# Performance work log

Hardware: AMD Instinct MI355X
Metric: run time of the kernel (lower is better)

## Reference

```python
import jax, jax.numpy as jnp
import numpy as np

B, C, H, W, NMAX = 16, 1, 128, 8192, 64


def setup_inputs() -> dict:
    key = jax.random.key(0)
    x = jax.random.normal(key, (B, C, H, W), dtype=jnp.float32)
    # Build realistic non-overlapping, sorted chirp boundaries with numpy.
    rng = np.random.default_rng(0)
    slot = W // NMAX  # 128 columns per chirp slot
    gaps = rng.integers(0, 40, size=(B, NMAX))
    widths = rng.integers(20, slot - 40, size=(B, NMAX))
    starts = np.arange(NMAX)[None, :] * slot + gaps
    ends = starts + widths
    n = rng.integers(48, NMAX + 1, size=(B,)).astype(np.int32)
    xi = np.stack([starts, ends], axis=-1).astype(np.int32)
    valid = np.arange(NMAX)[None, :] < n[:, None]
    xi = xi * valid[:, :, None]  # zero out invalid rows
    return {
        "x": x,
        "xi": jnp.asarray(xi),
        "N": jnp.asarray(n),
        "sep_param": jnp.zeros((1, 1, 1), dtype=jnp.float32),  # learned sep token scalar
    }


def reference(x, xi, N, sep_param):
    """Vectorized TinyBird.compactify_data: remove silence between chirp
    blocks, packing blocks contiguously with 1-column separators.
    Returns (x_new, xi_new). x_new keeps full width W (original truncates
    to data-dependent w_max; padding beyond w_max is zeros, same values)."""
    Bb, Cc, Hh, Ww = x.shape
    nmax = xi.shape[1]
    idx = jnp.arange(nmax, dtype=jnp.int32)[None, :]            # (1, Nmax)
    Nc = N.reshape(Bb, 1).astype(jnp.int32)                      # (B, 1)
    w = jnp.clip(xi[:, :, 1] - xi[:, :, 0], 0, None).astype(jnp.int32)
    valid = idx < Nc                                             # (B, Nmax)
    wv = jnp.where(valid, w, 0)
    csum = jnp.cumsum(wv, axis=1)
    start_new = csum - wv + idx                                  # compressed starts
    end_new = csum + idx                                         # compressed ends
    xi_new = jnp.where(valid[:, :, None],
                       jnp.stack([start_new, end_new], axis=-1), 0).astype(xi.dtype)

    # For every output column j, find which compressed segment it falls in.
    j = jnp.arange(Ww, dtype=jnp.int32)
    big = jnp.int32(Ww + nmax + 2)
    start_search = jnp.where(valid, start_new, big)              # keep sorted
    seg = jax.vmap(lambda s: jnp.searchsorted(s, j, side='right'))(start_search) - 1
    seg = jnp.clip(seg, 0, nmax - 1)                             # (B, W)
    bidx = jnp.arange(Bb)[:, None]
    s_new = start_new[bidx, seg]
    e_new = end_new[bidx, seg]
    seg_valid = valid[bidx, seg]
    in_seg = seg_valid & (j[None, :] >= s_new) & (j[None, :] < e_new)
    is_sep = seg_valid & (j[None, :] == e_new) & (seg < (Nc - 1))
    src = jnp.clip(xi[bidx, seg, 0].astype(jnp.int32) + (j[None, :] - s_new), 0, Ww - 1)
    src_full = jnp.broadcast_to(src[:, None, None, :], (Bb, Cc, Hh, Ww))
    gathered = jnp.take_along_axis(x, src_full, axis=3)          # ragged gather
    sep_val = sep_param[0, 0, 0]                                 # sep_token column value
    x_new = jnp.where(in_seg[:, None, None, :], gathered,
                      jnp.where(is_sep[:, None, None, :], sep_val, jnp.float32(0)))
    return x_new, xi_new
```

## Files before the change

kernel.cpp:

```cpp
#include <hip/hip_runtime.h>

#define Bn 16
#define Hn 128
#define Wn 8192
#define NMAX 64
#define TILE 1024
#define TPB 256

__global__ void xi_new_kernel(const int* __restrict__ xi,
                              const int* __restrict__ N,
                              float* __restrict__ out_xi) {
    int b = blockIdx.x;
    int i = threadIdx.x;
    int nb = N[b];
    int s0 = xi[(b * NMAX + i) * 2 + 0];
    int s1 = xi[(b * NMAX + i) * 2 + 1];
    int w = s1 - s0; if (w < 0) w = 0;
    bool valid = i < nb;
    int wv = valid ? w : 0;
    int c = wv;
    #pragma unroll
    for (int d = 1; d < 64; d <<= 1) {
        int t = __shfl_up(c, d, 64);
        if (i >= d) c += t;
    }
    int start_new = c - wv + i;
    int end_new = c + i;
    out_xi[(b * NMAX + i) * 2 + 0] = valid ? (float)start_new : 0.0f;
    out_xi[(b * NMAX + i) * 2 + 1] = valid ? (float)end_new : 0.0f;
}

__global__ __launch_bounds__(TPB) void compact_kernel(
    const float* __restrict__ x, const int* __restrict__ xi,
    const int* __restrict__ N, const float* __restrict__ sep_param,
    float* __restrict__ out) {
    __shared__ int s_start[NMAX];
    __shared__ int s_end[NMAX];
    __shared__ int s_src0[NMAX];
    __shared__ int s_n;

    const int blk  = blockIdx.x;
    const int tile = blk & 7;
    const int row  = blk >> 3;
    const int b    = row >> 7;
    const int tid  = threadIdx.x;

    if (tid < NMAX) {
        int nb = N[b];
        int s0 = xi[(b * NMAX + tid) * 2 + 0];
        int s1 = xi[(b * NMAX + tid) * 2 + 1];
        int w = s1 - s0; if (w < 0) w = 0;
        bool valid = tid < nb;
        int wv = valid ? w : 0;
        int c = wv;
        #pragma unroll
        for (int d = 1; d < 64; d <<= 1) {
            int t = __shfl_up(c, d, 64);
            if (tid >= d) c += t;
        }
        int start_new = c - wv + tid;
        int end_new = c + tid;
        s_start[tid] = valid ? start_new : 0x7FFFFFFF;
        s_end[tid]   = valid ? end_new : -1;
        s_src0[tid]  = s0;
        if (tid == 0) s_n = nb;
    }
    __syncthreads();

    const float sep = sep_param[0];
    const int nb = s_n;
    const float* __restrict__ xrow = x + (size_t)row * Wn;
    float* __restrict__ orow = out + (size_t)row * Wn;
    const int j0 = tile * TILE + tid * 4;

    float arr[4];
    #pragma unroll
    for (int k = 0; k < 4; ++k) {
        const int j = j0 + k;
        int seg = 0;
        #pragma unroll
        for (int step = 32; step > 0; step >>= 1) {
            int cand = seg + step;
            if (cand < NMAX && s_start[cand] <= j) seg = cand;
        }
        const int s = s_start[seg];
        const int e = s_end[seg];
        float val = 0.0f;
        if (j < e) {
            int src = s_src0[seg] + (j - s);
            if (src < 0) src = 0;
            if (src > Wn - 1) src = Wn - 1;
            val = xrow[src];
        } else if (j == e && seg < nb - 1) {
            val = sep;
        }
        arr[k] = val;
    }
    *reinterpret_cast<float4*>(orow + j0) = make_float4(arr[0], arr[1], arr[2], arr[3]);
}

extern "C" void kernel_launch(void* const* d_in, const int* in_sizes, int n_in,
                              void* d_out, int out_size, void* d_ws, size_t ws_size,
                              hipStream_t stream) {
    const float* x   = (const float*)d_in[0];
    const int* xi    = (const int*)d_in[1];
    const int* N     = (const int*)d_in[2];
    const float* sep = (const float*)d_in[3];

    float* out_x  = (float*)d_out;
    float* out_xi = (float*)d_out + (size_t)Bn * Hn * Wn;

    xi_new_kernel<<<Bn, NMAX, 0, stream>>>(xi, N, out_xi);

    const int blocks = Bn * Hn * (Wn / TILE);
    compact_kernel<<<blocks, TPB, 0, stream>>>(x, xi, N, sep, out_x);
}
```

Before: 137.3 us.

## Precompute per-batch source index map once, then run a lightweight row gather

A new code_kernel runs the segment scan and binary search once per batch element and per column. It writes an int map to workspace holding the source column, or a marker for separator or zero, and also emits xi_new. A gather_kernel then processes one full row per block, reading that map and gathering from x, so the per-row prefix scan, shared-memory setup, barrier and binary search are no longer repeated for each of the 128 rows. This adds a 512KB workspace round trip and a second launch, and falls back to the old path if the workspace is too small.

```diff
diff --git a/kernel.cpp b/kernel.cpp
--- a/kernel.cpp
+++ b/kernel.cpp
@@ -4,8 +4,170 @@
 #define Hn 128
 #define Wn 8192
 #define NMAX 64
-#define TILE 1024
-#define TPB 256
+
+__global__ __launch_bounds__(256) void code_kernel(
+    const int* __restrict__ xi, const int* __restrict__ N,
+    int* __restrict__ code, float* __restrict__ out_xi) {
+    __shared__ int s_start[NMAX];
+    __shared__ int s_end[NMAX];
+    __shared__ int s_src0[NMAX];
+    __shared__ int s_n;
+
+    const int b    = blockIdx.x >> 3;
+    const int tile = blockIdx.x & 7;
+    const int tid  = threadIdx.x;
+
+    if (tid < NMAX) {
+        int nb = N[b];
+        int s0 = xi[(b * NMAX + tid) * 2 + 0];
+        int s1 = xi[(b * NMAX + tid) * 2 + 1];
+        int w = s1 - s0; if (w < 0) w = 0;
+        bool valid = tid < nb;
+        int wv = valid ? w : 0;
+        int c = wv;
+        #pragma unroll
+        for (int d = 1; d < 64; d <<= 1) {
+            int t = __shfl_up(c, d, 64);
+            if (tid >= d) c += t;
+        }
+        int start_new = c - wv + tid;
+        int end_new = c + tid;
+        s_start[tid] = valid ? start_new : 0x7FFFFFFF;
+        s_end[tid]   = valid ? end_new : -1;
+        s_src0[tid]  = s0;
+        if (tid == 0) s_n = nb;
+        if (tile == 0) {
+            out_xi[(b * NMAX + tid) * 2 + 0] = valid ? (float)start_new : 0.0f;
+            out_xi[(b * NMAX + tid) * 2 + 1] = valid ? (float)end_new : 0.0f;
+        }
+    }
+    __syncthreads();
+
+    const int nb = s_n;
+    const int j0 = tile * 1024 + tid * 4;
+    int out4[4];
+    #pragma unroll
+    for (int k = 0; k < 4; ++k) {
+        const int j = j0 + k;
+        int seg = 0;
+        #pragma unroll
+        for (int step = 32; step > 0; step >>= 1) {
+            int cand = seg + step;
+            if (cand < NMAX && s_start[cand] <= j) seg = cand;
+        }
+        const int s = s_start[seg];
+        const int e = s_end[seg];
+        int c;
+        if (j < e) {
+            int src = s_src0[seg] + (j - s);
+            if (src < 0) src = 0;
+            if (src > Wn - 1) src = Wn - 1;
+            c = src;
+        } else if (j == e && seg < nb - 1) {
+            c = -2;
+        } else {
+            c = -1;
+        }
+        out4[k] = c;
+    }
+    *reinterpret_cast<int4*>(code + b * Wn + j0) =
+        make_int4(out4[0], out4[1], out4[2], out4[3]);
+}
+
+__global__ __launch_bounds__(256) void gather_kernel(
+    const float* __restrict__ x, const int* __restrict__ code,
+    const float* __restrict__ sep_param, float* __restrict__ out) {
+    const int row = blockIdx.x;
+    const int b   = row >> 7;
+    const int tid = threadIdx.x;
+
+    const float sep = sep_param[0];
+    const float* __restrict__ xrow = x + (size_t)row * Wn;
+    float* __restrict__ orow = out + (size_t)row * Wn;
+    const int* __restrict__ crow = code + b * Wn;
+
+    int4 c[8];
+    #pragma unroll
+    for (int g = 0; g < 8; ++g) {
+        c[g] = *reinterpret_cast<const int4*>(crow + g * 1024 + tid * 4);
+    }
+    #pragma unroll
+    for (int g = 0; g < 8; ++g) {
+        float4 v;
+        v.x = (c[g].x >= 0) ? xrow[c[g].x] : ((c[g].x == -2) ? sep : 0.0f);
+        v.y = (c[g].y >= 0) ? xrow[c[g].y] : ((c[g].y == -2) ? sep : 0.0f);
+        v.z = (c[g].z >= 0) ? xrow[c[g].z] : ((c[g].z == -2) ? sep : 0.0f);
+        v.w = (c[g].w >= 0) ? xrow[c[g].w] : ((c[g].w == -2) ? sep : 0.0f);
+        *reinterpret_cast<float4*>(orow + g * 1024 + tid * 4) = v;
+    }
+}
+
+__global__ __launch_bounds__(256) void compact_kernel(
+    const float* __restrict__ x, const int* __restrict__ xi,
+    const int* __restrict__ N, const float* __restrict__ sep_param,
+    float* __restrict__ out) {
+    __shared__ int s_start[NMAX];
+    __shared__ int s_end[NMAX];
+    __shared__ int s_src0[NMAX];
+    __shared__ int s_n;
+
+    const int blk  = blockIdx.x;
+    const int tile = blk & 7;
+    const int row  = blk >> 3;
+    const int b    = row >> 7;
+    const int tid  = threadIdx.x;
+
+    if (tid < NMAX) {
+        int nb = N[b];
+        int s0 = xi[(b * NMAX + tid) * 2 + 0];
+        int s1 = xi[(b * NMAX + tid) * 2 + 1];
+        int w = s1 - s0; if (w < 0) w = 0;
+        bool valid = tid < nb;
+        int wv = valid ? w : 0;
+        int c = wv;
+        #pragma unroll
+        for (int d = 1; d < 64; d <<= 1) {
+            int t = __shfl_up(c, d, 64);
+            if (tid >= d) c += t;
+        }
+        s_start[tid] = valid ? (c - wv + tid) : 0x7FFFFFFF;
+        s_end[tid]   = valid ? (c + tid) : -1;
+        s_src0[tid]  = s0;
+        if (tid == 0) s_n = nb;
+    }
+    __syncthreads();
+
+    const float sep = sep_param[0];
+    const int nb = s_n;
+    const float* __restrict__ xrow = x + (size_t)row * Wn;
+    float* __restrict__ orow = out + (size_t)row * Wn;
+    const int j0 = tile * 1024 + tid * 4;
+
+    float arr[4];
+    #pragma unroll
+    for (int k = 0; k < 4; ++k) {
+        const int j = j0 + k;
+        int seg = 0;
+        #pragma unroll
+        for (int step = 32; step > 0; step >>= 1) {
+            int cand = seg + step;
+            if (cand < NMAX && s_start[cand] <= j) seg = cand;
+        }
+        const int s = s_start[seg];
+        const int e = s_end[seg];
+        float val = 0.0f;
+        if (j < e) {
+            int src = s_src0[seg] + (j - s);
+            if (src < 0) src = 0;
+            if (src > Wn - 1) src = Wn - 1;
+            val = xrow[src];
+        } else if (j == e && seg < nb - 1) {
+            val = sep;
+        }
+        arr[k] = val;
+    }
+    *reinterpret_cast<float4*>(orow + j0) = make_float4(arr[0], arr[1], arr[2], arr[3]);
+}
 
 __global__ void xi_new_kernel(const int* __restrict__ xi,
                               const int* __restrict__ N,
@@ -24,79 +186,8 @@
         int t = __shfl_up(c, d, 64);
         if (i >= d) c += t;
     }
-    int start_new = c - wv + i;
-    int end_new = c + i;
-    out_xi[(b * NMAX + i) * 2 + 0] = valid ? (float)start_new : 0.0f;
-    out_xi[(b * NMAX + i) * 2 + 1] = valid ? (float)end_new : 0.0f;
-}
-
-__global__ __launch_bounds__(TPB) void compact_kernel(
-    const float* __restrict__ x, const int* __restrict__ xi,
-    const int* __restrict__ N, const float* __restrict__ sep_param,
-    float* __restrict__ out) {
-    __shared__ int s_start[NMAX];
-    __shared__ int s_end[NMAX];
-    __shared__ int s_src0[NMAX];
-    __shared__ int s_n;
-
-    const int blk  = blockIdx.x;
-    const int tile = blk & 7;
-    const int row  = blk >> 3;
-    const int b    = row >> 7;
-    const int tid  = threadIdx.x;
-
-    if (tid < NMAX) {
-        int nb = N[b];
-        int s0 = xi[(b * NMAX + tid) * 2 + 0];
-        int s1 = xi[(b * NMAX + tid) * 2 + 1];
-        int w = s1 - s0; if (w < 0) w = 0;
-        bool valid = tid < nb;
-        int wv = valid ? w : 0;
-        int c = wv;
-        #pragma unroll
-        for (int d = 1; d < 64; d <<= 1) {
-            int t = __shfl_up(c, d, 64);
-            if (tid >= d) c += t;
-        }
-        int start_new = c - wv + tid;
-        int end_new = c + tid;
-        s_start[tid] = valid ? start_new : 0x7FFFFFFF;
-        s_end[tid]   = valid ? end_new : -1;
-        s_src0[tid]  = s0;
-        if (tid == 0) s_n = nb;
-    }
-    __syncthreads();
-
-    const float sep = sep_param[0];
-    const int nb = s_n;
-    const float* __restrict__ xrow = x + (size_t)row * Wn;
-    float* __restrict__ orow = out + (size_t)row * Wn;
-    const int j0 = tile * TILE + tid * 4;
-
-    float arr[4];
-    #pragma unroll
-    for (int k = 0; k < 4; ++k) {
-        const int j = j0 + k;
-        int seg = 0;
-        #pragma unroll
-        for (int step = 32; step > 0; step >>= 1) {
-            int cand = seg + step;
-            if (cand < NMAX && s_start[cand] <= j) seg = cand;
-        }
-        const int s = s_start[seg];
-        const int e = s_end[seg];
-        float val = 0.0f;
-        if (j < e) {
-            int src = s_src0[seg] + (j - s);
-            if (src < 0) src = 0;
-            if (src > Wn - 1) src = Wn - 1;
-            val = xrow[src];
-        } else if (j == e && seg < nb - 1) {
-            val = sep;
-        }
-        arr[k] = val;
-    }
-    *reinterpret_cast<float4*>(orow + j0) = make_float4(arr[0], arr[1], arr[2], arr[3]);
+    out_xi[(b * NMAX + i) * 2 + 0] = valid ? (float)(c - wv + i) : 0.0f;
+    out_xi[(b * NMAX + i) * 2 + 1] = valid ? (float)(c + i) : 0.0f;
 }
 
 extern "C" void kernel_launch(void* const* d_in, const int* in_sizes, int n_in,
@@ -110,8 +201,13 @@
     float* out_x  = (float*)d_out;
     float* out_xi = (float*)d_out + (size_t)Bn * Hn * Wn;
 
-    xi_new_kernel<<<Bn, NMAX, 0, stream>>>(xi, N, out_xi);
-
-    const int blocks = Bn * Hn * (Wn / TILE);
-    compact_kernel<<<blocks, TPB, 0, stream>>>(x, xi, N, sep, out_x);
-}
+    const size_t code_bytes = (size_t)Bn * Wn * sizeof(int);
+    if (ws_size >= code_bytes) {
+        int* code = (int*)d_ws;
+        code_kernel<<<Bn * 8, 256, 0, stream>>>(xi, N, code, out_xi);
+        gather_kernel<<<Bn * Hn, 256, 0, stream>>>(x, code, sep, out_x);
+    } else {
+        xi_new_kernel<<<Bn, NMAX, 0, stream>>>(xi, N, out_xi);
+        compact_kernel<<<Bn * Hn * 8, 256, 0, stream>>>(x, xi, N, sep, out_x);
+    }
+}
```

New measurement: 123.1 us. -10.4%, faster.

## Replace per-column binary search with per-segment copy loop and nontemporal zero tail

Applied to the files above, without the earlier changes.

Switches from a gather-style kernel, where each output column binary-searches its segment, to a scatter-style kernel. One block handles a whole row, each wave copies whole segments plus their separator, and the zero tail past the last segment is written with vectorized nontemporal stores. This removes the per-element search and reads only the source columns that are needed. In exchange, segment copies are scalar and unaligned, lanes sit idle on short segments, and parallelism drops to one block per row. The source-index clamp is gone, so correctness assumes in-range inputs.

```diff
diff --git a/kernel.cpp b/kernel.cpp
--- a/kernel.cpp
+++ b/kernel.cpp
@@ -4,8 +4,8 @@
 #define Hn 128
 #define Wn 8192
 #define NMAX 64
-#define TILE 1024
-#define TPB 256
+
+typedef float nt_f4 __attribute__((ext_vector_type(4)));
 
 __global__ void xi_new_kernel(const int* __restrict__ xi,
                               const int* __restrict__ N,
@@ -24,26 +24,22 @@
         int t = __shfl_up(c, d, 64);
         if (i >= d) c += t;
     }
-    int start_new = c - wv + i;
-    int end_new = c + i;
-    out_xi[(b * NMAX + i) * 2 + 0] = valid ? (float)start_new : 0.0f;
-    out_xi[(b * NMAX + i) * 2 + 1] = valid ? (float)end_new : 0.0f;
+    out_xi[(b * NMAX + i) * 2 + 0] = valid ? (float)(c - wv + i) : 0.0f;
+    out_xi[(b * NMAX + i) * 2 + 1] = valid ? (float)(c + i) : 0.0f;
 }
 
-__global__ __launch_bounds__(TPB) void compact_kernel(
+__global__ __launch_bounds__(256) void row_copy_kernel(
     const float* __restrict__ x, const int* __restrict__ xi,
     const int* __restrict__ N, const float* __restrict__ sep_param,
     float* __restrict__ out) {
     __shared__ int s_start[NMAX];
-    __shared__ int s_end[NMAX];
+    __shared__ int s_w[NMAX];
     __shared__ int s_src0[NMAX];
-    __shared__ int s_n;
+    __shared__ int s_n, s_tail;
 
-    const int blk  = blockIdx.x;
-    const int tile = blk & 7;
-    const int row  = blk >> 3;
-    const int b    = row >> 7;
-    const int tid  = threadIdx.x;
+    const int row = blockIdx.x;
+    const int b   = row >> 7;
+    const int tid = threadIdx.x;
 
     if (tid < NMAX) {
         int nb = N[b];
@@ -59,44 +55,42 @@
             if (tid >= d) c += t;
         }
         int start_new = c - wv + tid;
-        int end_new = c + tid;
-        s_start[tid] = valid ? start_new : 0x7FFFFFFF;
-        s_end[tid]   = valid ? end_new : -1;
+        int end_new   = c + tid;
+        s_start[tid] = start_new;
+        s_w[tid]     = wv;
         s_src0[tid]  = s0;
         if (tid == 0) s_n = nb;
+        int last = (nb > 0) ? (nb - 1) : 0;
+        if (tid == last) s_tail = (nb > 0) ? end_new : 0;
     }
     __syncthreads();
 
+    const int nb   = s_n;
+    const int tail = s_tail;
     const float sep = sep_param[0];
-    const int nb = s_n;
     const float* __restrict__ xrow = x + (size_t)row * Wn;
     float* __restrict__ orow = out + (size_t)row * Wn;
-    const int j0 = tile * TILE + tid * 4;
+    const int wave = tid >> 6;
+    const int lane = tid & 63;
 
-    float arr[4];
-    #pragma unroll
-    for (int k = 0; k < 4; ++k) {
-        const int j = j0 + k;
-        int seg = 0;
-        #pragma unroll
-        for (int step = 32; step > 0; step >>= 1) {
-            int cand = seg + step;
-            if (cand < NMAX && s_start[cand] <= j) seg = cand;
+    for (int seg = wave; seg < nb; seg += 4) {
+        const int s    = s_start[seg];
+        const int w    = s_w[seg];
+        const int src0 = s_src0[seg];
+        const int wtot = w + (seg < nb - 1 ? 1 : 0);
+        for (int l = lane; l < wtot; l += 64) {
+            float v = (l < w) ? xrow[src0 + l] : sep;
+            orow[s + l] = v;
         }
-        const int s = s_start[seg];
-        const int e = s_end[seg];
-        float val = 0.0f;
-        if (j < e) {
-            int src = s_src0[seg] + (j - s);
-            if (src < 0) src = 0;
-            if (src > Wn - 1) src = Wn - 1;
-            val = xrow[src];
-        } else if (j == e && seg < nb - 1) {
-            val = sep;
-        }
-        arr[k] = val;
     }
-    *reinterpret_cast<float4*>(orow + j0) = make_float4(arr[0], arr[1], arr[2], arr[3]);
+
+    const int t4 = (tail + 3) & ~3;
+    if (tid < (t4 - tail)) orow[tail + tid] = 0.0f;
+    const nt_f4 z = {0.0f, 0.0f, 0.0f, 0.0f};
+    nt_f4* orow4 = reinterpret_cast<nt_f4*>(orow);
+    for (int i4 = (t4 >> 2) + tid; i4 < (Wn >> 2); i4 += 256) {
+        __builtin_nontemporal_store(z, orow4 + i4);
+    }
 }
 
 extern "C" void kernel_launch(void* const* d_in, const int* in_sizes, int n_in,
@@ -111,7 +105,5 @@
     float* out_xi = (float*)d_out + (size_t)Bn * Hn * Wn;
 
     xi_new_kernel<<<Bn, NMAX, 0, stream>>>(xi, N, out_xi);
-
-    const int blocks = Bn * Hn * (Wn / TILE);
-    compact_kernel<<<blocks, TPB, 0, stream>>>(x, xi, N, sep, out_x);
+    row_copy_kernel<<<Bn * Hn, 256, 0, stream>>>(x, xi, N, sep, out_x);
 }
```

Result: faster. 127.7 us (-7.0%).
